# Optimization experiments

Measured on AMD Instinct MI355X. Metric: run time of the kernel, lower is better.

The kernel has to match this reference:

```python
import jax, jax.numpy as jnp
import numpy as np

B, T, N1, K = 128, 512, 512, 8   # batch, steps, n_customers+1, knn_k
CAPACITY = 50.0
NEG_INF = -1e9


def setup_inputs() -> dict:
    key = jax.random.key(0)
    k0, k1, k2, k3, k4, k5 = jax.random.split(key, 6)
    psi_prime = jax.random.normal(k0, (B, N1, 2), dtype=jnp.float32)
    demands = jax.random.uniform(k1, (B, N1), dtype=jnp.float32) * 9.0 + 1.0
    demands = demands.at[:, 0].set(0.0)  # depot has zero demand
    actions = jax.random.randint(k2, (B, T), 0, N1, dtype=jnp.int32)
    knn_indices = jax.random.randint(k3, (B, N1, K), 0, N1, dtype=jnp.int32)
    Wq_w = jax.random.normal(k4, (2, 4), dtype=jnp.float32) * 0.5
    Wq_b = jax.random.normal(k5, (2,), dtype=jnp.float32) * 0.1
    lambda_param = jnp.float32(0.1)
    return {"psi_prime": psi_prime, "demands": demands, "Wq_w": Wq_w,
            "Wq_b": Wq_b, "lambda_param": lambda_param,
            "actions": actions, "knn_indices": knn_indices}


def _rollout_states(demands, actions):
    """Reconstruct the T per-step states (cur, used, vis) BEFORE each action."""
    mb, Tn = actions.shape
    n1 = demands.shape[1]
    batch = jnp.arange(mb)

    def step(carry, act_t):
        cur, used, vis = carry
        out = (cur, used, vis)  # record state before applying act_t
        at_depot = act_t == 0
        dem_t = jnp.take_along_axis(demands, act_t[:, None], axis=1)[:, 0]
        used_n = jnp.where(at_depot, 0.0, used + dem_t)
        vis_n = vis.at[batch, act_t].set(True)
        vis_n = vis_n.at[:, 0].set(False)
        return (act_t, used_n, vis_n), out

    init = (jnp.zeros((mb,), jnp.int32), jnp.zeros((mb,), jnp.float32),
            jnp.zeros((mb, n1), dtype=bool))
    _, (all_cur, all_used, all_vis) = jax.lax.scan(step, init, actions.T)
    # scan stacks over leading T axis -> move batch first
    return all_cur.T, all_used.T, jnp.transpose(all_vis, (1, 0, 2))


def _evaluate(psi_prime, demands, Wq_w, Wq_b, lambda_param, actions, knn_indices):
    mb, Tn = actions.shape
    n_cust = psi_prime.shape[1] - 1

    all_cur, all_used, all_vis = _rollout_states(demands, actions)  # [B,T],[B,T],[B,T,N1]

    remaining = CAPACITY - all_used                      # [B,T]
    cap_norm = remaining / max(CAPACITY, 1e-8)
    exceeds = demands[:, None, :] > remaining[:, :, None]  # [B,T,N1]
    mask = all_vis | exceeds
    mask = mask.at[:, :, 0].set(False)
    at_depot = all_cur == 0                               # [B,T]
    has_cust = jnp.any(~mask[:, :, 1:], axis=-1)
    mask = mask.at[:, :, 0].set(at_depot & has_cust)

    psi_curr = jnp.take_along_axis(psi_prime, all_cur[:, :, None], axis=1)  # [B,T,2]
    psi_curr = jnp.where(at_depot[:, :, None], 0.0, psi_curr)
    t_norm = jnp.arange(Tn, dtype=jnp.float32) / max(n_cust, 1)
    t_norm = jnp.broadcast_to(t_norm[None, :], (mb, Tn))
    ctx = jnp.concatenate([psi_curr, cap_norm[:, :, None], t_norm[:, :, None]], axis=-1)  # [B,T,4]

    query = ctx @ Wq_w.T + Wq_b                           # [B,T,2]
    context_scores = jnp.einsum('btd,bnd->btn', query, psi_prime)  # [B,T,N1]

    # kNN interference: per-node dot with its k nearest neighbours, summed
    neigh = psi_prime[jnp.arange(mb)[:, None, None], knn_indices]  # [B,N1,K,2]
    interf = jnp.einsum('bnd,bnkd->bn', psi_prime, neigh)          # [B,N1]

    scores = context_scores + lambda_param * interf[:, None, :]
    scores = jnp.where(mask, NEG_INF, scores)
    log_probs = jax.nn.log_softmax(scores, axis=-1)                # [B,T,N1]

    lp_new = jnp.take_along_axis(log_probs, actions[:, :, None], axis=2)[:, :, 0]  # [B,T]
    ent = -jnp.sum(jnp.exp(log_probs) * log_probs, axis=-1)        # [B,T]
    entropy = ent.mean(axis=1)                                     # [B]
    return lp_new, entropy


def reference(psi_prime, demands, Wq_w, Wq_b, lambda_param, actions, knn_indices):
    return _evaluate(psi_prime, demands, Wq_w, Wq_b, lambda_param, actions, knn_indices)
```

## Files before the change

### kernel.cpp

```cpp
#include <hip/hip_runtime.h>
#include <hip/hip_bf16.h>

#define B_  128
#define T_  512
#define N1_ 512
#define K_  8
#define CAPf 50.0f
#define NEG_INF_F (-1000000000.0f)
#define NEG_INF_L2 (-1442695040.0f)
#define L2E  1.44269504088896341f
#define LN2  0.69314718055994531f

__device__ __forceinline__ int   fi(float x) { return __float_as_int(x); }
__device__ __forceinline__ float uf(int x)   { return __int_as_float(x); }

__device__ __forceinline__ float wave_sum64(float x) {
    x += uf(__builtin_amdgcn_update_dpp(0, fi(x), 0x111, 0xF, 0xF, true));
    x += uf(__builtin_amdgcn_update_dpp(0, fi(x), 0x112, 0xF, 0xF, true));
    x += uf(__builtin_amdgcn_update_dpp(0, fi(x), 0x114, 0xF, 0xF, true));
    x += uf(__builtin_amdgcn_update_dpp(0, fi(x), 0x118, 0xF, 0xF, true));
    x += uf(__builtin_amdgcn_update_dpp(0, fi(x), 0x142, 0xA, 0xF, true));
    x += uf(__builtin_amdgcn_update_dpp(0, fi(x), 0x143, 0xC, 0xF, true));
    return uf(__builtin_amdgcn_readlane(fi(x), 63));
}
__device__ __forceinline__ float wave_max64_pos(float x) {
    x = fmaxf(x, uf(__builtin_amdgcn_update_dpp(0, fi(x), 0x111, 0xF, 0xF, true)));
    x = fmaxf(x, uf(__builtin_amdgcn_update_dpp(0, fi(x), 0x112, 0xF, 0xF, true)));
    x = fmaxf(x, uf(__builtin_amdgcn_update_dpp(0, fi(x), 0x114, 0xF, 0xF, true)));
    x = fmaxf(x, uf(__builtin_amdgcn_update_dpp(0, fi(x), 0x118, 0xF, 0xF, true)));
    x = fmaxf(x, uf(__builtin_amdgcn_update_dpp(0, fi(x), 0x142, 0xA, 0xF, true)));
    x = fmaxf(x, uf(__builtin_amdgcn_update_dpp(0, fi(x), 0x143, 0xC, 0xF, true)));
    return uf(__builtin_amdgcn_readlane(fi(x), 63));
}

__global__ __launch_bounds__(256) void prep_kernel(
    const float* __restrict__ psi,
    const float* __restrict__ demands,
    const float* __restrict__ lambda_p,
    const int*   __restrict__ actions,
    const int*   __restrict__ knn,
    float4* __restrict__ ws_pk,
    int*    __restrict__ ws_fv,
    float*  __restrict__ ws_used)
{
    __shared__ float2 psi_l[N1_];
    __shared__ float  dem_l[N1_];
    __shared__ int    fv_l[N1_];
    __shared__ int    act_l[T_];
    __shared__ float2 md_l[T_];

    const int b   = blockIdx.x;
    const int tid = threadIdx.x;

    const float2* psi2 = (const float2*)psi;
    for (int i = tid; i < N1_; i += 256) {
        psi_l[i] = psi2[b * N1_ + i];
        dem_l[i] = demands[b * N1_ + i];
        fv_l[i]  = 0x7fffffff;
    }
    for (int t = tid; t < T_; t += 256) act_l[t] = actions[b * T_ + t];
    __syncthreads();

    for (int t = tid; t < T_; t += 256) {
        int a = act_l[t];
        atomicMin(&fv_l[a], t);
        float d = dem_l[a];
        md_l[t] = (a == 0) ? make_float2(0.0f, 0.0f) : make_float2(1.0f, d);
    }
    __syncthreads();

    if (tid == 0) {
        float u = 0.0f;
        #pragma unroll 8
        for (int t = 0; t < T_; ++t) {
            ws_used[b * T_ + t] = u;
            float2 md = md_l[t];
            u = fmaf(md.x, u, md.y);
        }
    } else if (tid >= 64) {
        const float lam = (*lambda_p) * L2E;
        for (int n = tid - 64; n < N1_; n += 192) {
            float2 p = psi_l[n];
            const int4* kk = (const int4*)(knn + ((size_t)b * N1_ + n) * K_);
            int4 k0 = kk[0], k1 = kk[1];
            int ks[8] = {k0.x, k0.y, k0.z, k0.w, k1.x, k1.y, k1.z, k1.w};
            float acc = 0.0f;
            #pragma unroll
            for (int k = 0; k < 8; ++k) {
                float2 q = psi_l[ks[k]];
                acc = fmaf(p.x, q.x, acc);
                acc = fmaf(p.y, q.y, acc);
            }
            ws_pk[b * N1_ + n] = make_float4(p.x, p.y, lam * acc, dem_l[n]);
        }
    }
    __syncthreads();
    for (int n = tid; n < N1_; n += 256) ws_fv[b * N1_ + n] = fv_l[n];
}

__global__ __launch_bounds__(256, 4) void main_kernel(
    const float*  __restrict__ Wq_w,
    const float*  __restrict__ Wq_b,
    const int*    __restrict__ actions,
    const float4* __restrict__ ws_pk,
    const int*    __restrict__ ws_fv,
    const float*  __restrict__ ws_used,
    float* __restrict__ out_lp,
    float* __restrict__ out_ent)
{
    __shared__ float used_s[32];
    __shared__ int   act_s[33];
    __shared__ float went[4];

    const int bid    = blockIdx.x;
    const int b      = bid >> 4;
    const int chunk  = bid & 15;
    const int t_base = chunk * 32;
    const int tid    = threadIdx.x;
    const int wave   = tid >> 6;
    const int lane   = tid & 63;

    if (tid < 32) used_s[tid] = ws_used[b * T_ + t_base + tid];
    if (tid < 33) {
        int tt = t_base - 1 + tid;
        act_s[tid] = (tt < 0) ? 0 : actions[b * T_ + tt];
    }

    float4 pk[8];
    int    fvr[8];
    #pragma unroll
    for (int j = 0; j < 8; ++j) {
        pk[j]  = ws_pk[b * N1_ + j * 64 + lane];
        fvr[j] = ws_fv[b * N1_ + j * 64 + lane];
    }
    const float W00 = Wq_w[0], W01 = Wq_w[1], W02 = Wq_w[2], W03 = Wq_w[3];
    const float W10 = Wq_w[4], W11 = Wq_w[5], W12 = Wq_w[6], W13 = Wq_w[7];
    const float bq0 = Wq_b[0], bq1 = Wq_b[1];
    __syncthreads();

    float ent_acc = 0.0f;

    #pragma unroll 1
    for (int rr = 0; rr < 4; ++rr) {
        const int iA = wave * 8 + rr * 2;
        const int iB = iA + 1;
        const int tA = t_base + iA;
        const int tB = t_base + iB;
        const int curA = (tA == 0) ? 0 : act_s[iA];
        const int curB = act_s[iB];
        const int aA = act_s[iA + 1];
        const int aB = act_s[iB + 1];
        const float remA = CAPf - used_s[iA];
        const float remB = CAPf - used_s[iB];
        const bool depA = (curA == 0);
        const bool depB = (curB == 0);

        float4 pcA = ws_pk[b * N1_ + curA];
        float4 pcB = ws_pk[b * N1_ + curB];
        const float pcxA = depA ? 0.0f : pcA.x, pcyA = depA ? 0.0f : pcA.y;
        const float pcxB = depB ? 0.0f : pcB.x, pcyB = depB ? 0.0f : pcB.y;

        const float capA = remA * (1.0f / CAPf), capB = remB * (1.0f / CAPf);
        const float tnA = (float)tA * (1.0f / 511.0f);
        const float tnB = (float)tB * (1.0f / 511.0f);

        const float q0A = fmaf(pcxA, W00, fmaf(pcyA, W01, fmaf(capA, W02, fmaf(tnA, W03, bq0)))) * L2E;
        const float q1A = fmaf(pcxA, W10, fmaf(pcyA, W11, fmaf(capA, W12, fmaf(tnA, W13, bq1)))) * L2E;
        const float q0B = fmaf(pcxB, W00, fmaf(pcyB, W01, fmaf(capB, W02, fmaf(tnB, W03, bq0)))) * L2E;
        const float q1B = fmaf(pcxB, W10, fmaf(pcyB, W11, fmaf(capB, W12, fmaf(tnB, W13, bq1)))) * L2E;

        float sA[8], sB[8];
        bool avA = false, avB = false;
        #pragma unroll
        for (int j = 0; j < 8; ++j) {
            const int n = j * 64 + lane;
            float scA = fmaf(q0A, pk[j].x, fmaf(q1A, pk[j].y, pk[j].z));
            float scB = fmaf(q0B, pk[j].x, fmaf(q1B, pk[j].y, pk[j].z));
            if (n != 0) {
                bool mA = (fvr[j] < tA) | (pk[j].w > remA);
                bool mB = (fvr[j] < tB) | (pk[j].w > remB);
                avA |= !mA;  avB |= !mB;
                scA = mA ? NEG_INF_L2 : scA;
                scB = mB ? NEG_INF_L2 : scB;
            }
            sA[j] = scA;  sB[j] = scB;
        }

        const bool hasA = __any((int)avA);
        const bool hasB = __any((int)avB);
        if (lane == 0 && depA && hasA) sA[0] = NEG_INF_L2;
        if (lane == 0 && depB && hasB) sB[0] = NEG_INF_L2;

        float preA = fmaxf(fmaxf(fmaxf(sA[0], sA[1]), fmaxf(sA[2], sA[3])),
                           fmaxf(fmaxf(sA[4], sA[5]), fmaxf(sA[6], sA[7])));
        float preB = fmaxf(fmaxf(fmaxf(sB[0], sB[1]), fmaxf(sB[2], sB[3])),
                           fmaxf(fmaxf(sB[4], sB[5]), fmaxf(sB[6], sB[7])));
        const float mxA = wave_max64_pos(preA + 2048.0f) - 2048.0f;
        const float mxB = wave_max64_pos(preB + 2048.0f) - 2048.0f;

        float S1A = 0.0f, S2A = 0.0f, S1B = 0.0f, S2B = 0.0f;
        #pragma unroll
        for (int j = 0; j < 8; ++j) {
            float eA = __builtin_amdgcn_exp2f(sA[j] - mxA);
            float eB = __builtin_amdgcn_exp2f(sB[j] - mxB);
            S1A += eA;  S2A = fmaf(eA, sA[j], S2A);
            S1B += eB;  S2B = fmaf(eB, sB[j], S2B);
        }
        S1A = wave_sum64(S1A);  S2A = wave_sum64(S2A);
        S1B = wave_sum64(S1B);  S2B = wave_sum64(S2B);

        const float lgA = __builtin_amdgcn_logf(S1A);
        const float lgB = __builtin_amdgcn_logf(S1B);

        const int jaA = aA >> 6, jaB = aB >> 6;
        float svA = sA[0], svB = sB[0];
        svA = (jaA == 1) ? sA[1] : svA;  svB = (jaB == 1) ? sB[1] : svB;
        svA = (jaA == 2) ? sA[2] : svA;  svB = (jaB == 2) ? sB[2] : svB;
        svA = (jaA == 3) ? sA[3] : svA;  svB = (jaB == 3) ? sB[3] : svB;
        svA = (jaA == 4) ? sA[4] : svA;  svB = (jaB == 4) ? sB[4] : svB;
        svA = (jaA == 5) ? sA[5] : svA;  svB = (jaB == 5) ? sB[5] : svB;
        svA = (jaA == 6) ? sA[6] : svA;  svB = (jaB == 6) ? sB[6] : svB;
        svA = (jaA == 7) ? sA[7] : svA;  svB = (jaB == 7) ? sB[7] : svB;
        const float s_aA = uf(__builtin_amdgcn_readlane(fi(svA), aA & 63));
        const float s_aB = uf(__builtin_amdgcn_readlane(fi(svB), aB & 63));

        if (lane == 0) {
            out_lp[b * T_ + tA] = LN2 * ((s_aA - mxA) - lgA);
            out_lp[b * T_ + tB] = LN2 * ((s_aB - mxB) - lgB);
        }
        ent_acc += ((mxA + lgA) - __fdividef(S2A, S1A))
                 + ((mxB + lgB) - __fdividef(S2B, S1B));
    }

    if (lane == 0) went[wave] = ent_acc;
    __syncthreads();
    if (tid == 0) {
        float s = (went[0] + went[1]) + (went[2] + went[3]);
        atomicAdd(&out_ent[b], s * (LN2 / 512.0f));
    }
}

extern "C" void kernel_launch(void* const* d_in, const int* in_sizes, int n_in,
                              void* d_out, int out_size, void* d_ws, size_t ws_size,
                              hipStream_t stream) {
    const float* psi      = (const float*)d_in[0];
    const float* demands  = (const float*)d_in[1];
    const float* Wq_w     = (const float*)d_in[2];
    const float* Wq_b     = (const float*)d_in[3];
    const float* lam      = (const float*)d_in[4];
    const int*   actions  = (const int*)d_in[5];
    const int*   knn      = (const int*)d_in[6];

    float* out_lp  = (float*)d_out;
    float* out_ent = out_lp + (size_t)B_ * T_;

    float4* ws_pk  = (float4*)d_ws;
    int*    ws_fv  = (int*)  ((char*)d_ws + (size_t)B_ * N1_ * 16);
    float*  ws_used= (float*)((char*)d_ws + (size_t)B_ * N1_ * 20);

    prep_kernel<<<B_, 256, 0, stream>>>(psi, demands, lam, actions, knn,
                                        ws_pk, ws_fv, ws_used);
    main_kernel<<<B_ * 16, 256, 0, stream>>>(Wq_w, Wq_b, actions,
                                             ws_pk, ws_fv, ws_used,
                                             out_lp, out_ent);
}
```

Before: 99.61 us.

## Stage per-batch node data in LDS and use 512-thread blocks per batch quarter

The main kernel now stages each batch's packed node data and first-visit times in shared memory, instead of holding them in registers that every 32-step block reloads from global memory. Blocks grow to 512 threads covering 128 steps each, so the grid shrinks from 2048 to 512 blocks and per-batch global reloads drop fourfold. The inner loop now reads node data from LDS every iteration, adding LDS traffic and shared-memory footprint. The smaller grid may also reduce latency hiding on a many-CU GPU.

```diff
diff --git a/kernel.cpp b/kernel.cpp
--- a/kernel.cpp
+++ b/kernel.cpp
@@ -98,7 +98,7 @@
     for (int n = tid; n < N1_; n += 256) ws_fv[b * N1_ + n] = fv_l[n];
 }
 
-__global__ __launch_bounds__(256, 4) void main_kernel(
+__global__ __launch_bounds__(512) void main_kernel(
     const float*  __restrict__ Wq_w,
     const float*  __restrict__ Wq_b,
     const int*    __restrict__ actions,
@@ -108,30 +108,28 @@
     float* __restrict__ out_lp,
     float* __restrict__ out_ent)
 {
-    __shared__ float used_s[32];
-    __shared__ int   act_s[33];
-    __shared__ float went[4];
-
-    const int bid    = blockIdx.x;
-    const int b      = bid >> 4;
-    const int chunk  = bid & 15;
-    const int t_base = chunk * 32;
-    const int tid    = threadIdx.x;
-    const int wave   = tid >> 6;
-    const int lane   = tid & 63;
-
-    if (tid < 32) used_s[tid] = ws_used[b * T_ + t_base + tid];
-    if (tid < 33) {
+    __shared__ float4 pk_l[N1_];
+    __shared__ int    fv_l[N1_];
+    __shared__ float  used_s[128];
+    __shared__ int    act_s[129];
+    __shared__ float  went[8];
+
+    const int bid     = blockIdx.x;
+    const int b       = bid >> 2;
+    const int quarter = bid & 3;
+    const int t_base  = quarter * 128;
+    const int tid     = threadIdx.x;
+    const int wave    = tid >> 6;
+    const int lane    = tid & 63;
+
+    if (tid < N1_) {
+        pk_l[tid] = ws_pk[b * N1_ + tid];
+        fv_l[tid] = ws_fv[b * N1_ + tid];
+    }
+    if (tid < 128) used_s[tid] = ws_used[b * T_ + t_base + tid];
+    if (tid < 129) {
         int tt = t_base - 1 + tid;
         act_s[tid] = (tt < 0) ? 0 : actions[b * T_ + tt];
-    }
-
-    float4 pk[8];
-    int    fvr[8];
-    #pragma unroll
-    for (int j = 0; j < 8; ++j) {
-        pk[j]  = ws_pk[b * N1_ + j * 64 + lane];
-        fvr[j] = ws_fv[b * N1_ + j * 64 + lane];
     }
     const float W00 = Wq_w[0], W01 = Wq_w[1], W02 = Wq_w[2], W03 = Wq_w[3];
     const float W10 = Wq_w[4], W11 = Wq_w[5], W12 = Wq_w[6], W13 = Wq_w[7];
@@ -141,8 +139,8 @@
     float ent_acc = 0.0f;
 
     #pragma unroll 1
-    for (int rr = 0; rr < 4; ++rr) {
-        const int iA = wave * 8 + rr * 2;
+    for (int rr = 0; rr < 8; ++rr) {
+        const int iA = wave * 16 + rr * 2;
         const int iB = iA + 1;
         const int tA = t_base + iA;
         const int tB = t_base + iB;
@@ -155,8 +153,8 @@
         const bool depA = (curA == 0);
         const bool depB = (curB == 0);
 
-        float4 pcA = ws_pk[b * N1_ + curA];
-        float4 pcB = ws_pk[b * N1_ + curB];
+        float4 pcA = pk_l[curA];
+        float4 pcB = pk_l[curB];
         const float pcxA = depA ? 0.0f : pcA.x, pcyA = depA ? 0.0f : pcA.y;
         const float pcxB = depB ? 0.0f : pcB.x, pcyB = depB ? 0.0f : pcB.y;
 
@@ -174,11 +172,13 @@
         #pragma unroll
         for (int j = 0; j < 8; ++j) {
             const int n = j * 64 + lane;
-            float scA = fmaf(q0A, pk[j].x, fmaf(q1A, pk[j].y, pk[j].z));
-            float scB = fmaf(q0B, pk[j].x, fmaf(q1B, pk[j].y, pk[j].z));
+            const float4 P = pk_l[n];
+            const int   fv = fv_l[n];
+            float scA = fmaf(q0A, P.x, fmaf(q1A, P.y, P.z));
+            float scB = fmaf(q0B, P.x, fmaf(q1B, P.y, P.z));
             if (n != 0) {
-                bool mA = (fvr[j] < tA) | (pk[j].w > remA);
-                bool mB = (fvr[j] < tB) | (pk[j].w > remB);
+                bool mA = (fv < tA) | (P.w > remA);
+                bool mB = (fv < tB) | (P.w > remB);
                 avA |= !mA;  avB |= !mB;
                 scA = mA ? NEG_INF_L2 : scA;
                 scB = mB ? NEG_INF_L2 : scB;
@@ -235,7 +235,8 @@
     if (lane == 0) went[wave] = ent_acc;
     __syncthreads();
     if (tid == 0) {
-        float s = (went[0] + went[1]) + (went[2] + went[3]);
+        float s = ((went[0] + went[1]) + (went[2] + went[3]))
+                + ((went[4] + went[5]) + (went[6] + went[7]));
         atomicAdd(&out_ent[b], s * (LN2 / 512.0f));
     }
 }
@@ -260,7 +261,7 @@
 
     prep_kernel<<<B_, 256, 0, stream>>>(psi, demands, lam, actions, knn,
                                         ws_pk, ws_fv, ws_used);
-    main_kernel<<<B_ * 16, 256, 0, stream>>>(Wq_w, Wq_b, actions,
-                                             ws_pk, ws_fv, ws_used,
-                                             out_lp, out_ent);
-}
+    main_kernel<<<B_ * 4, 512, 0, stream>>>(Wq_w, Wq_b, actions,
+                                            ws_pk, ws_fv, ws_used,
+                                            out_lp, out_ent);
+}
```

Result: faster. 97.24 us (-2.4%).
